# Kernel tuning notes

Hardware: AMD Instinct MI355X
Metric: run time of the kernel (lower is better)

Reference implementation:

```python
import jax, jax.numpy as jnp
import numpy as np

N_NODES, N_EDGES = 50000, 800000
N_IN, E_IN, N_OUT, E_OUT = 64, 32, 64, 32


def _xavier(key, fan_in, fan_out):
    std = (2.0 / (fan_in + fan_out)) ** 0.5
    return jax.random.normal(key, (fan_in, fan_out), dtype=jnp.float32) * std


def setup_inputs() -> dict:
    key = jax.random.key(0)
    ks = jax.random.split(key, 10)
    return {
        "feat": jax.random.normal(ks[0], (N_NODES, N_IN), dtype=jnp.float32),
        "edge_feat": jax.random.normal(ks[1], (N_EDGES, E_IN), dtype=jnp.float32),
        "w_msg": _xavier(ks[2], N_IN + E_IN, N_OUT),
        "b_msg": jnp.zeros((N_OUT,), dtype=jnp.float32),
        "w_node": _xavier(ks[3], N_IN + N_OUT, N_OUT),
        "b_node": jnp.zeros((N_OUT,), dtype=jnp.float32),
        "w_edge": _xavier(ks[4], N_IN + N_OUT + E_IN, E_OUT),
        "b_edge": jnp.zeros((E_OUT,), dtype=jnp.float32),
        "src_idx": jax.random.randint(ks[5], (N_EDGES,), 0, N_NODES, dtype=jnp.int32),
        "dst_idx": jax.random.randint(ks[6], (N_EDGES,), 0, N_NODES, dtype=jnp.int32),
    }


def reference(feat, edge_feat, w_msg, b_msg, w_node, b_node, w_edge, b_edge, src_idx, dst_idx):
    n_nodes = feat.shape[0]
    # --- message: gather src + edge, linear, tanh --- [E, n_out]
    src_h = feat[src_idx]
    m = jnp.tanh(jnp.concatenate([src_h, edge_feat], axis=1) @ w_msg + b_msg)
    # --- scatter-mean into destination nodes --- [N, n_out]
    sums = jax.ops.segment_sum(m, dst_idx, num_segments=n_nodes)
    cnt = jax.ops.segment_sum(jnp.ones((m.shape[0], 1), m.dtype), dst_idx, num_segments=n_nodes)
    neigh = sums / jnp.maximum(cnt, 1.0)
    # --- node update: cat([neigh, h]) -> linear -> tanh (dropout = identity in eval) ---
    h = jnp.tanh(jnp.concatenate([neigh, feat], axis=1) @ w_node + b_node)
    # --- edge update: cat([src h, dst neigh(updated), edge h]) -> linear -> tanh ---
    e = jnp.tanh(jnp.concatenate([src_h, h[dst_idx], edge_feat], axis=1) @ w_edge + b_edge)
    return h, e
```

## Files before the change

### kernel.cpp

```cpp
#include <hip/hip_runtime.h>

#define NNODES 50000
#define NEDGES 800000
#define NPAD   50176
#define NTILE_E (NEDGES / 16)
#define NTILE_N (NNODES / 16)

typedef __attribute__((ext_vector_type(8))) short bf16x8;
typedef __attribute__((ext_vector_type(4))) float f32x4;

union ABu { bf16x8 v; uint4 u; };

__device__ __forceinline__ float fast_tanh(float x) {
    float e = __expf(2.0f * x);
    return 1.0f - 2.0f * __builtin_amdgcn_rcpf(e + 1.0f);
}

__device__ __forceinline__ unsigned pk_rne(float x, float y) {
    unsigned a = __float_as_uint(x), b = __float_as_uint(y);
    a = (a + 0x7fffu + ((a >> 16) & 1u)) >> 16;
    b = (b + 0x7fffu + ((b >> 16) & 1u)) >> 16;
    return a | (b << 16);
}
__device__ __forceinline__ unsigned pk_tr(float a, float b) {
    return __builtin_amdgcn_perm(__float_as_uint(b), __float_as_uint(a), 0x07060302);
}
__device__ __forceinline__ float bf16_lo(unsigned u) { return __uint_as_float(u << 16); }
__device__ __forceinline__ float bf16_hi(unsigned u) { return __uint_as_float(u & 0xffff0000u); }

__device__ __forceinline__ ABu make_afrag(const float* p) {
    float4 a = ((const float4*)p)[0];
    float4 b = ((const float4*)p)[1];
    ABu r;
    r.u.x = pk_tr(a.x, a.y); r.u.y = pk_tr(a.z, a.w);
    r.u.z = pk_tr(b.x, b.y); r.u.w = pk_tr(b.z, b.w);
    return r;
}

template <int LDN>
__device__ __forceinline__ ABu make_bfrag_u(const unsigned* wp) {
    ABu r;
    r.u.x = wp[0 * LDN]; r.u.y = wp[1 * LDN];
    r.u.z = wp[2 * LDN]; r.u.w = wp[3 * LDN];
    return r;
}

template <int KH, int N>
__device__ __forceinline__ void stage_w(const float* __restrict__ w, unsigned* wl_u) {
    for (int i = threadIdx.x; i < KH * N; i += 256) {
        const int kp = i / N, n = i % N;
        wl_u[i] = pk_rne(w[(2 * kp) * N + n], w[(2 * kp + 1) * N + n]);
    }
}

#define MFMA(a, b, c) __builtin_amdgcn_mfma_f32_16x16x32_bf16((a).v, (b).v, (c), 0, 0, 0)

__global__ __launch_bounds__(256) void hist_kernel(const int* __restrict__ dst_idx,
                                                   int* __restrict__ cnt,
                                                   int* __restrict__ rank) {
    const int base = (blockIdx.x * 256 + threadIdx.x) * 4;
    if (base + 4 <= NEDGES) {
        int4 d = *(const int4*)(dst_idx + base);
        int4 r;
        r.x = atomicAdd(&cnt[d.x], 1);
        r.y = atomicAdd(&cnt[d.y], 1);
        r.z = atomicAdd(&cnt[d.z], 1);
        r.w = atomicAdd(&cnt[d.w], 1);
        *(int4*)(rank + base) = r;
    } else {
        for (int i = base; i < NEDGES; ++i) rank[i] = atomicAdd(&cnt[dst_idx[i]], 1);
    }
}

__global__ __launch_bounds__(256) void scan1(const int* __restrict__ cnt,
                                             int* __restrict__ off,
                                             int* __restrict__ btot) {
    __shared__ int s[256];
    const int tid = threadIdx.x;
    const int g = blockIdx.x * 256 + tid;
    const int own = cnt[g];
    s[tid] = own;
    __syncthreads();
    for (int o = 1; o < 256; o <<= 1) {
        int v = (tid >= o) ? s[tid - o] : 0;
        __syncthreads();
        s[tid] += v;
        __syncthreads();
    }
    off[g] = s[tid] - own;
    if (tid == 255) btot[blockIdx.x] = s[255];
}

__global__ __launch_bounds__(256) void scan2(int* __restrict__ btot) {
    __shared__ int s[256];
    const int tid = threadIdx.x;
    const int own = btot[tid];
    s[tid] = own;
    __syncthreads();
    for (int o = 1; o < 256; o <<= 1) {
        int v = (tid >= o) ? s[tid - o] : 0;
        __syncthreads();
        s[tid] += v;
        __syncthreads();
    }
    btot[tid] = s[tid] - own;
}

__global__ __launch_bounds__(256) void scan3(int* __restrict__ off,
                                             const int* __restrict__ btot) {
    const int g = blockIdx.x * 256 + threadIdx.x;
    off[g] += btot[blockIdx.x];
}

template <int KC, int NT>
__global__ __launch_bounds__(256) void proj_kernel(
    const float* __restrict__ in, const float* __restrict__ w,
    const float* __restrict__ bias, float* __restrict__ out) {
    constexpr int N = NT * 16;
    constexpr int K = KC * 32;
    __shared__ __align__(16) unsigned wl[(K / 2) * N];
    stage_w<K / 2, N>(w, wl);
    __syncthreads();

    const int lane = threadIdx.x & 63, wave = threadIdx.x >> 6;
    const int col = lane & 15, quad = lane >> 4;

    ABu bf[KC][NT];
#pragma unroll
    for (int kc = 0; kc < KC; ++kc)
#pragma unroll
        for (int nt = 0; nt < NT; ++nt)
            bf[kc][nt] = make_bfrag_u<N>(&wl[(kc * 16 + (quad << 2)) * N + nt * 16 + col]);

    float bi[NT];
#pragma unroll
    for (int nt = 0; nt < NT; ++nt) bi[nt] = bias ? bias[nt * 16 + col] : 0.f;

    const int nw = gridDim.x << 2;
    for (int t = (blockIdx.x << 2) + wave; t < NTILE_N; t += nw) {
        const int n0 = t << 4;
        const int n = n0 + col;
        ABu a[KC];
#pragma unroll
        for (int kc = 0; kc < KC; ++kc)
            a[kc] = make_afrag(in + (size_t)n * K + kc * 32 + (quad << 3));

        f32x4 acc[NT];
#pragma unroll
        for (int nt = 0; nt < NT; ++nt)
            acc[nt] = (f32x4){bi[nt], bi[nt], bi[nt], bi[nt]};
#pragma unroll
        for (int nt = 0; nt < NT; ++nt)
#pragma unroll
            for (int kc = 0; kc < KC; ++kc)
                acc[nt] = MFMA(a[kc], bf[kc][nt], acc[nt]);

#pragma unroll
        for (int i = 0; i < 4; ++i) {
            const int nr = n0 + (quad << 2) + i;
            if (NT == 4) {
                float4 o = {acc[0][i], acc[1][i], acc[2][i], acc[3][i]};
                *(float4*)(out + (size_t)nr * 64 + (col << 2)) = o;
            } else {
                float2 o = {acc[0][i], acc[1][i]};
                *(float2*)(out + (size_t)nr * 32 + (col << 1)) = o;
            }
        }
    }
}

struct MsgBuf { ABu a2; float4 f4[4]; int4 rows; };

__device__ __forceinline__ void msg_load(
    int t, int col, int quad,
    const float* __restrict__ edge_feat, const float* __restrict__ projm,
    const int* __restrict__ src_idx, const int* __restrict__ dst_idx,
    const int* __restrict__ off, const int* __restrict__ rank, MsgBuf& b) {
    const int e0 = t << 4;
    const int4 s4 = *(const int4*)(src_idx + e0 + (quad << 2));
    const int4 d4 = *(const int4*)(dst_idx + e0 + (quad << 2));
    const int4 r4 = *(const int4*)(rank + e0 + (quad << 2));
    b.rows.x = off[d4.x] + r4.x;
    b.rows.y = off[d4.y] + r4.y;
    b.rows.z = off[d4.z] + r4.z;
    b.rows.w = off[d4.w] + r4.w;
    b.a2 = make_afrag(edge_feat + (size_t)(e0 + col) * 32 + (quad << 3));
    b.f4[0] = *(const float4*)(projm + (size_t)s4.x * 64 + (col << 2));
    b.f4[1] = *(const float4*)(projm + (size_t)s4.y * 64 + (col << 2));
    b.f4[2] = *(const float4*)(projm + (size_t)s4.z * 64 + (col << 2));
    b.f4[3] = *(const float4*)(projm + (size_t)s4.w * 64 + (col << 2));
}

__device__ __forceinline__ void msg_comp(
    int col, const ABu (&bf)[4], const MsgBuf& b, unsigned* __restrict__ m_out) {
    f32x4 acc[4];
#pragma unroll
    for (int nt = 0; nt < 4; ++nt) acc[nt] = (f32x4){0.f, 0.f, 0.f, 0.f};
#pragma unroll
    for (int nt = 0; nt < 4; ++nt) acc[nt] = MFMA(b.a2, bf[nt], acc[nt]);
    const int rw[4] = {b.rows.x, b.rows.y, b.rows.z, b.rows.w};
#pragma unroll
    for (int i = 0; i < 4; ++i) {
        uint2 o;
        o.x = pk_rne(fast_tanh(acc[0][i] + b.f4[i].x), fast_tanh(acc[1][i] + b.f4[i].y));
        o.y = pk_rne(fast_tanh(acc[2][i] + b.f4[i].z), fast_tanh(acc[3][i] + b.f4[i].w));
        *(uint2*)(m_out + (size_t)rw[i] * 32 + (col << 1)) = o;
    }
}

__global__ __launch_bounds__(256) void msg_kernel(
    const float* __restrict__ edge_feat, const float* __restrict__ w_bot,
    const int* __restrict__ src_idx, const int* __restrict__ dst_idx,
    const int* __restrict__ off, const int* __restrict__ rank,
    const float* __restrict__ projm, unsigned* __restrict__ m_out) {
    __shared__ __align__(16) unsigned wl[16 * 64];
    stage_w<16, 64>(w_bot, wl);
    __syncthreads();

    const int lane = threadIdx.x & 63, wave = threadIdx.x >> 6;
    const int col = lane & 15, quad = lane >> 4;

    ABu bf[4];
#pragma unroll
    for (int nt = 0; nt < 4; ++nt)
        bf[nt] = make_bfrag_u<64>(&wl[(quad << 2) * 64 + nt * 16 + col]);

    const int nw = gridDim.x << 2;
    int t = (blockIdx.x << 2) + wave;
    if (t >= NTILE_E) return;
    MsgBuf A, B;
    msg_load(t, col, quad, edge_feat, projm, src_idx, dst_idx, off, rank, A);
    for (;;) {
        const int t2 = t + nw;
        if (t2 < NTILE_E)
            msg_load(t2, col, quad, edge_feat, projm, src_idx, dst_idx, off, rank, B);
        msg_comp(col, bf, A, m_out);
        if (t2 >= NTILE_E) return;
        const int t3 = t2 + nw;
        if (t3 < NTILE_E)
            msg_load(t3, col, quad, edge_feat, projm, src_idx, dst_idx, off, rank, A);
        msg_comp(col, bf, B, m_out);
        if (t3 >= NTILE_E) return;
        t = t3;
    }
}

__global__ __launch_bounds__(256) void gather_kernel(
    const unsigned* __restrict__ m,
    const int* __restrict__ off , const int* __restrict__ cnt,
    float* __restrict__ neigh) {
    const int wave = threadIdx.x >> 6;
    const int lane = threadIdx.x & 63;
    const int n = blockIdx.x * 4 + wave;
    if (n >= NNODES) return;
    const int c = cnt[n];
    const int o = off[n];
    const int q = lane & 7;
    const int g = lane >> 3;

    float s[8];
#pragma unroll
    for (int j = 0; j < 8; ++j) s[j] = 0.f;
    for (int r = g; r < c; r += 8) {
        const uint4 u = *(const uint4*)(m + (size_t)(o + r) * 32 + (q << 2));
        s[0] += bf16_lo(u.x); s[1] += bf16_hi(u.x);
        s[2] += bf16_lo(u.y); s[3] += bf16_hi(u.y);
        s[4] += bf16_lo(u.z); s[5] += bf16_hi(u.z);
        s[6] += bf16_lo(u.w); s[7] += bf16_hi(u.w);
    }
#pragma unroll
    for (int j = 0; j < 8; ++j) {
        s[j] += __shfl_xor(s[j], 8);
        s[j] += __shfl_xor(s[j], 16);
        s[j] += __shfl_xor(s[j], 32);
    }
    if (g == 0) {
        const float inv = __builtin_amdgcn_rcpf((float)max(c, 1));
        float4 o0 = {s[0] * inv, s[1] * inv, s[2] * inv, s[3] * inv};
        float4 o1 = {s[4] * inv, s[5] * inv, s[6] * inv, s[7] * inv};
        float* dst = neigh + (size_t)n * 64 + (q << 3);
        ((float4*)dst)[0] = o0;
        ((float4*)dst)[1] = o1;
    }
}

__device__ __forceinline__ int mapk(int ks) {
    return ks < 64 ? ((ks >> 2) + ((ks >> 1) & 1) * 32 + (ks & 1) * 16) : ks;
}

__global__ __launch_bounds__(256) void node_update(
    const float* __restrict__ feat,
    const float* __restrict__ w_node, const float* __restrict__ b_node,
    float* __restrict__ h) {
    __shared__ __align__(16) float wl[128 * 64];
    for (int i = threadIdx.x; i < 128 * 64; i += 256) wl[i] = w_node[i];
    __syncthreads();

    const int lane = threadIdx.x & 63, wave = threadIdx.x >> 6;
    const int col = lane & 15, quad = lane >> 4;

    ABu bf[4][4];
#pragma unroll
    for (int kc = 0; kc < 4; ++kc)
#pragma unroll
        for (int nt = 0; nt < 4; ++nt) {
            unsigned p[4];
#pragma unroll
            for (int jj = 0; jj < 4; ++jj) {
                const int k0 = kc * 32 + quad * 8 + jj * 2;
                p[jj] = pk_rne(wl[mapk(k0) * 64 + nt * 16 + col],
                               wl[mapk(k0 + 1) * 64 + nt * 16 + col]);
            }
            bf[kc][nt].u = (uint4){p[0], p[1], p[2], p[3]};
        }

    float bias[4];
#pragma unroll
    for (int nt = 0; nt < 4; ++nt) bias[nt] = b_node[nt * 16 + col];

    const int nw = gridDim.x << 2;
    for (int t = (blockIdx.x << 2) + wave; t < NTILE_N; t += nw) {
        const int n0 = t << 4;
        const int n = n0 + col;
        ABu a0 = make_afrag(h + (size_t)n * 64 + quad * 8);
        ABu a1 = make_afrag(h + (size_t)n * 64 + 32 + quad * 8);
        ABu a2 = make_afrag(feat + (size_t)n * 64 + quad * 8);
        ABu a3 = make_afrag(feat + (size_t)n * 64 + 32 + quad * 8);

        f32x4 acc[4];
#pragma unroll
        for (int nt = 0; nt < 4; ++nt)
            acc[nt] = (f32x4){bias[nt], bias[nt], bias[nt], bias[nt]};
#pragma unroll
        for (int nt = 0; nt < 4; ++nt) {
            acc[nt] = MFMA(a0, bf[0][nt], acc[nt]);
            acc[nt] = MFMA(a1, bf[1][nt], acc[nt]);
            acc[nt] = MFMA(a2, bf[2][nt], acc[nt]);
            acc[nt] = MFMA(a3, bf[3][nt], acc[nt]);
        }
#pragma unroll
        for (int i = 0; i < 4; ++i) {
            const int nr = n0 + quad * 4 + i;
#pragma unroll
            for (int nt = 0; nt < 4; ++nt)
                h[(size_t)nr * 64 + nt * 16 + col] = fast_tanh(acc[nt][i]);
        }
    }
}

struct EBuf { ABu a4; float2 g1[4]; float2 g2[4]; };

__device__ __forceinline__ void edge_load(
    int t, int col, int quad,
    const float* __restrict__ edge_feat,
    const float* __restrict__ p1, const float* __restrict__ p2,
    const int* __restrict__ src_idx, const int* __restrict__ dst_idx, EBuf& b) {
    const int e0 = t << 4;
    const int4 s4 = *(const int4*)(src_idx + e0 + (quad << 2));
    const int4 d4 = *(const int4*)(dst_idx + e0 + (quad << 2));
    b.a4 = make_afrag(edge_feat + (size_t)(e0 + col) * 32 + (quad << 3));
    b.g1[0] = *(const float2*)(p1 + (size_t)s4.x * 32 + (col << 1));
    b.g1[1] = *(const float2*)(p1 + (size_t)s4.y * 32 + (col << 1));
    b.g1[2] = *(const float2*)(p1 + (size_t)s4.z * 32 + (col << 1));
    b.g1[3] = *(const float2*)(p1 + (size_t)s4.w * 32 + (col << 1));
    b.g2[0] = *(const float2*)(p2 + (size_t)d4.x * 32 + (col << 1));
    b.g2[1] = *(const float2*)(p2 + (size_t)d4.y * 32 + (col << 1));
    b.g2[2] = *(const float2*)(p2 + (size_t)d4.z * 32 + (col << 1));
    b.g2[3] = *(const float2*)(p2 + (size_t)d4.w * 32 + (col << 1));
}

__device__ __forceinline__ void edge_comp(
    int t, int col, int quad, const ABu (&bf)[2],
    const EBuf& b, float* __restrict__ e_out) {
    f32x4 acc[2];
#pragma unroll
    for (int nt = 0; nt < 2; ++nt) acc[nt] = (f32x4){0.f, 0.f, 0.f, 0.f};
#pragma unroll
    for (int nt = 0; nt < 2; ++nt) acc[nt] = MFMA(b.a4, bf[nt], acc[nt]);
    const int e0 = t << 4;
#pragma unroll
    for (int i = 0; i < 4; ++i) {
        const int er = e0 + (quad << 2) + i;
        e_out[(size_t)er * 32 + col] = fast_tanh(acc[0][i] + b.g1[i].x + b.g2[i].x);
        e_out[(size_t)er * 32 + 16 + col] = fast_tanh(acc[1][i] + b.g1[i].y + b.g2[i].y);
    }
}

__global__ __launch_bounds__(256) void edge_update(
    const float* __restrict__ edge_feat, const float* __restrict__ w3,
    const float* __restrict__ p1, const float* __restrict__ p2,
    const int* __restrict__ src_idx, const int* __restrict__ dst_idx,
    float* __restrict__ e_out) {
    __shared__ __align__(16) unsigned wl[16 * 32];
    stage_w<16, 32>(w3, wl);
    __syncthreads();

    const int lane = threadIdx.x & 63, wave = threadIdx.x >> 6;
    const int col = lane & 15, quad = lane >> 4;

    ABu bf[2];
#pragma unroll
    for (int nt = 0; nt < 2; ++nt)
        bf[nt] = make_bfrag_u<32>(&wl[(quad << 2) * 32 + nt * 16 + col]);

    const int nw = gridDim.x << 2;
    int t = (blockIdx.x << 2) + wave;
    if (t >= NTILE_E) return;
    EBuf A, B;
    edge_load(t, col, quad, edge_feat, p1, p2, src_idx, dst_idx, A);
    for (;;) {
        const int t2 = t + nw;
        if (t2 < NTILE_E)
            edge_load(t2, col, quad, edge_feat, p1, p2, src_idx, dst_idx, B);
        edge_comp(t, col, quad, bf, A, e_out);
        if (t2 >= NTILE_E) return;
        const int t3 = t2 + nw;
        if (t3 < NTILE_E)
            edge_load(t3, col, quad, edge_feat, p1, p2, src_idx, dst_idx, A);
        edge_comp(t2, col, quad, bf, B, e_out);
        if (t3 >= NTILE_E) return;
        t = t3;
    }
}

extern "C" void kernel_launch(void* const* d_in, const int* in_sizes, int n_in,
                              void* d_out, int out_size, void* d_ws, size_t ws_size,
                              hipStream_t stream) {
    const float* feat      = (const float*)d_in[0];
    const float* edge_feat = (const float*)d_in[1];
    const float* w_msg     = (const float*)d_in[2];
    const float* b_msg     = (const float*)d_in[3];
    const float* w_node    = (const float*)d_in[4];
    const float* b_node    = (const float*)d_in[5];
    const float* w_edge    = (const float*)d_in[6];
    const float* b_edge    = (const float*)d_in[7];
    const int*   src_idx   = (const int*)d_in[8];
    const int*   dst_idx   = (const int*)d_in[9];

    float* h = (float*)d_out;
    float* e = (float*)d_out + (size_t)NNODES * 64;
    unsigned* m = (unsigned*)e;
    float* projm = h;

    int* cnt  = (int*)d_ws;
    int* off  = cnt + NPAD;
    int* btot = off + NPAD;
    int* rank = btot + 256;
    float* p1 = (float*)(rank + NEDGES);
    float* p2 = p1 + (size_t)NNODES * 32;

    hipMemsetAsync(cnt, 0, NPAD * sizeof(int), stream);
    hipMemsetAsync(btot, 0, 256 * sizeof(int), stream);

    hist_kernel<<<(NEDGES / 4 + 255) / 256, 256, 0, stream>>>(dst_idx, cnt, rank);
    scan1<<<NPAD / 256, 256, 0, stream>>>(cnt, off, btot);
    scan2<<<1, 256, 0, stream>>>(btot);
    scan3<<<NPAD / 256, 256, 0, stream>>>(off, btot);
    proj_kernel<2, 4><<<256, 256, 0, stream>>>(feat, w_msg, b_msg, projm);
    msg_kernel<<<1280, 256, 0, stream>>>(edge_feat, w_msg + 64 * 64,
                                         src_idx, dst_idx, off, rank, projm, m);
    gather_kernel<<<NNODES / 4, 256, 0, stream>>>(m, off, cnt, h);
    node_update<<<512, 256, 0, stream>>>(feat, w_node, b_node, h);
    proj_kernel<2, 2><<<256, 256, 0, stream>>>(feat, w_edge, b_edge, p1);
    proj_kernel<2, 2><<<256, 256, 0, stream>>>(h, w_edge + 64 * 32, nullptr, p2);
    edge_update<<<1280, 256, 0, stream>>>(edge_feat, w_edge + 128 * 32,
                                          p1, p2, src_idx, dst_idx, e);
}
```

Baseline: 390.2 us.

## Precompute scatter rows in separate kernel, prepack node weights, enlarge grids

Adds a rows_kernel that folds off[dst] into rank once, so msg_kernel loads a single int4 of destination rows instead of dst_idx, rank and a dependent gather of off. node_update now packs its weights to bf16 pairs in shared memory during staging, which halves the LDS footprint and simplifies fragment building. The grid sizes of msg_kernel and edge_update rise from 1280 to 2500 blocks. The trade-off is one extra kernel launch and an extra pass over the rank array.

Result: no change. 392.5 us (+0.6%).

```diff
diff --git a/kernel.cpp b/kernel.cpp
--- a/kernel.cpp
+++ b/kernel.cpp
@@ -112,6 +112,23 @@
     off[g] += btot[blockIdx.x];
 }
 
+__global__ __launch_bounds__(256) void rows_kernel(const int* __restrict__ dst_idx,
+                                                   const int* __restrict__ off,
+                                                   int* __restrict__ rank) {
+    const int base = (blockIdx.x * 256 + threadIdx.x) * 4;
+    if (base + 4 <= NEDGES) {
+        int4 d = *(const int4*)(dst_idx + base);
+        int4 r = *(const int4*)(rank + base);
+        r.x += off[d.x];
+        r.y += off[d.y];
+        r.z += off[d.z];
+        r.w += off[d.w];
+        *(int4*)(rank + base) = r;
+    } else {
+        for (int i = base; i < NEDGES; ++i) rank[i] += off[dst_idx[i]];
+    }
+}
+
 template <int KC, int NT>
 __global__ __launch_bounds__(256) void proj_kernel(
     const float* __restrict__ in, const float* __restrict__ w,
@@ -174,16 +191,10 @@
 __device__ __forceinline__ void msg_load(
     int t, int col, int quad,
     const float* __restrict__ edge_feat, const float* __restrict__ projm,
-    const int* __restrict__ src_idx, const int* __restrict__ dst_idx,
-    const int* __restrict__ off, const int* __restrict__ rank, MsgBuf& b) {
+    const int* __restrict__ src_idx, const int* __restrict__ rows, MsgBuf& b) {
     const int e0 = t << 4;
     const int4 s4 = *(const int4*)(src_idx + e0 + (quad << 2));
-    const int4 d4 = *(const int4*)(dst_idx + e0 + (quad << 2));
-    const int4 r4 = *(const int4*)(rank + e0 + (quad << 2));
-    b.rows.x = off[d4.x] + r4.x;
-    b.rows.y = off[d4.y] + r4.y;
-    b.rows.z = off[d4.z] + r4.z;
-    b.rows.w = off[d4.w] + r4.w;
+    b.rows = *(const int4*)(rows + e0 + (quad << 2));
     b.a2 = make_afrag(edge_feat + (size_t)(e0 + col) * 32 + (quad << 3));
     b.f4[0] = *(const float4*)(projm + (size_t)s4.x * 64 + (col << 2));
     b.f4[1] = *(const float4*)(projm + (size_t)s4.y * 64 + (col << 2));
@@ -210,8 +221,7 @@
 
 __global__ __launch_bounds__(256) void msg_kernel(
     const float* __restrict__ edge_feat, const float* __restrict__ w_bot,
-    const int* __restrict__ src_idx, const int* __restrict__ dst_idx,
-    const int* __restrict__ off, const int* __restrict__ rank,
+    const int* __restrict__ src_idx, const int* __restrict__ rows,
     const float* __restrict__ projm, unsigned* __restrict__ m_out) {
     __shared__ __align__(16) unsigned wl[16 * 64];
     stage_w<16, 64>(w_bot, wl);
@@ -229,16 +239,16 @@
     int t = (blockIdx.x << 2) + wave;
     if (t >= NTILE_E) return;
     MsgBuf A, B;
-    msg_load(t, col, quad, edge_feat, projm, src_idx, dst_idx, off, rank, A);
+    msg_load(t, col, quad, edge_feat, projm, src_idx, rows, A);
     for (;;) {
         const int t2 = t + nw;
         if (t2 < NTILE_E)
-            msg_load(t2, col, quad, edge_feat, projm, src_idx, dst_idx, off, rank, B);
+            msg_load(t2, col, quad, edge_feat, projm, src_idx, rows, B);
         msg_comp(col, bf, A, m_out);
         if (t2 >= NTILE_E) return;
         const int t3 = t2 + nw;
         if (t3 < NTILE_E)
-            msg_load(t3, col, quad, edge_feat, projm, src_idx, dst_idx, off, rank, A);
+            msg_load(t3, col, quad, edge_feat, projm, src_idx, rows, A);
         msg_comp(col, bf, B, m_out);
         if (t3 >= NTILE_E) return;
         t = t3;
@@ -292,8 +302,11 @@
     const float* __restrict__ feat,
     const float* __restrict__ w_node, const float* __restrict__ b_node,
     float* __restrict__ h) {
-    __shared__ __align__(16) float wl[128 * 64];
-    for (int i = threadIdx.x; i < 128 * 64; i += 256) wl[i] = w_node[i];
+    __shared__ __align__(16) unsigned wl[64 * 64];
+    for (int i = threadIdx.x; i < 64 * 64; i += 256) {
+        const int kp = i >> 6, n = i & 63;
+        wl[i] = pk_rne(w_node[mapk(2 * kp) * 64 + n], w_node[mapk(2 * kp + 1) * 64 + n]);
+    }
     __syncthreads();
 
     const int lane = threadIdx.x & 63, wave = threadIdx.x >> 6;
@@ -303,16 +316,8 @@
 #pragma unroll
     for (int kc = 0; kc < 4; ++kc)
 #pragma unroll
-        for (int nt = 0; nt < 4; ++nt) {
-            unsigned p[4];
-#pragma unroll
-            for (int jj = 0; jj < 4; ++jj) {
-                const int k0 = kc * 32 + quad * 8 + jj * 2;
-                p[jj] = pk_rne(wl[mapk(k0) * 64 + nt * 16 + col],
-                               wl[mapk(k0 + 1) * 64 + nt * 16 + col]);
-            }
-            bf[kc][nt].u = (uint4){p[0], p[1], p[2], p[3]};
-        }
+        for (int nt = 0; nt < 4; ++nt)
+            bf[kc][nt] = make_bfrag_u<64>(&wl[(kc * 16 + (quad << 2)) * 64 + nt * 16 + col]);
 
     float bias[4];
 #pragma unroll
@@ -456,13 +461,14 @@
     scan1<<<NPAD / 256, 256, 0, stream>>>(cnt, off, btot);
     scan2<<<1, 256, 0, stream>>>(btot);
     scan3<<<NPAD / 256, 256, 0, stream>>>(off, btot);
+    rows_kernel<<<(NEDGES / 4 + 255) / 256, 256, 0, stream>>>(dst_idx, off, rank);
     proj_kernel<2, 4><<<256, 256, 0, stream>>>(feat, w_msg, b_msg, projm);
-    msg_kernel<<<1280, 256, 0, stream>>>(edge_feat, w_msg + 64 * 64,
-                                         src_idx, dst_idx, off, rank, projm, m);
+    msg_kernel<<<2500, 256, 0, stream>>>(edge_feat, w_msg + 64 * 64,
+                                         src_idx, rank, projm, m);
     gather_kernel<<<NNODES / 4, 256, 0, stream>>>(m, off, cnt, h);
     node_update<<<512, 256, 0, stream>>>(feat, w_node, b_node, h);
     proj_kernel<2, 2><<<256, 256, 0, stream>>>(feat, w_edge, b_edge, p1);
     proj_kernel<2, 2><<<256, 256, 0, stream>>>(h, w_edge + 64 * 32, nullptr, p2);
-    edge_update<<<1280, 256, 0, stream>>>(edge_feat, w_edge + 128 * 32,
+    edge_update<<<2500, 256, 0, stream>>>(edge_feat, w_edge + 128 * 32,
                                           p1, p2, src_idx, dst_idx, e);
 }
```
